# Kernel optimization log

Measured on AMD Instinct MI355X. Metric: run time of the kernel, lower is better.

The kernel has to match this reference:

```python
import jax, jax.numpy as jnp
import numpy as np

D_MODEL = 256
G_CH = 512
N_HEADS = 8
EPS = 1e-6


def setup_inputs() -> dict:
    key0 = jax.random.key(0)
    ks = jax.random.split(key0, 24)
    B, N1, C, G = 2, 65536, D_MODEL, G_CH
    p = 0.05
    inp = {
        'query': jax.random.normal(ks[0], (B, N1, G), jnp.float32),
        'key': jax.random.normal(ks[1], (B, N1, C), jnp.float32),
        'value': jax.random.normal(ks[2], (B, N1, C), jnp.float32),
        # Mheads1: Linear(guidance_channels, d_model, bias=False); stored as [in,out]
        'mheads1_w': jax.random.normal(ks[3], (G, C), jnp.float32) * p,
        # CrossAttentionLayer q/k/v: Linear(d_model, d_model)
        'q_w': jax.random.normal(ks[4], (C, C), jnp.float32) * p,
        'q_b': jax.random.normal(ks[5], (C,), jnp.float32) * p,
        'k_w': jax.random.normal(ks[6], (C, C), jnp.float32) * p,
        'k_b': jax.random.normal(ks[7], (C,), jnp.float32) * p,
        'v_w': jax.random.normal(ks[8], (C, C), jnp.float32) * p,
        'v_b': jax.random.normal(ks[9], (C,), jnp.float32) * p,
        # MSCW local_attn: Linear->ReLU->Linear
        'l1_w': jax.random.normal(ks[10], (C, C), jnp.float32) * p,
        'l1_b': jax.random.normal(ks[11], (C,), jnp.float32) * p,
        'l2_w': jax.random.normal(ks[12], (C, C), jnp.float32) * p,
        'l2_b': jax.random.normal(ks[13], (C,), jnp.float32) * p,
        # MSCW global_attn: Linear->ReLU->Linear
        'g1_w': jax.random.normal(ks[14], (C, C), jnp.float32) * p,
        'g1_b': jax.random.normal(ks[15], (C,), jnp.float32) * p,
        'g2_w': jax.random.normal(ks[16], (C, C), jnp.float32) * p,
        'g2_b': jax.random.normal(ks[17], (C,), jnp.float32) * p,
    }
    return inp


def _haar_pool(feat):
    # feat: [B, C, H, W]; standard WCT2 WavePool: depthwise 2x2 stride-2 Haar conv.
    B, C, H, W = feat.shape
    x = feat.reshape(B, C, H // 2, 2, W // 2, 2)
    a = x[:, :, :, 0, :, 0]
    b = x[:, :, :, 0, :, 1]
    c = x[:, :, :, 1, :, 0]
    d = x[:, :, :, 1, :, 1]
    # Haar: L=[1,1]/sqrt2, Hf=[-1,1]/sqrt2 -> outer-product 2x2 filters, /2 overall
    LL = (a + b + c + d) * 0.5
    LH = (-a + b - c + d) * 0.5
    HL = (-a - b + c + d) * 0.5
    HH = (a - b - c + d) * 0.5
    return LL, LH, HL, HH


def reference(query, key, value, mheads1_w, q_w, q_b, k_w, k_b, v_w, v_b,
              l1_w, l1_b, l2_w, l2_b, g1_w, g1_b, g2_w, g2_b):
    B, n1, C = value.shape
    hw = int(round(n1 ** 0.5))
    q_guid = query @ mheads1_w  # [B, L, C]

    feat = jnp.transpose(key, (0, 2, 1)).reshape(B, C, hw, hw)
    LL, LH, HL, HH = _haar_pool(feat)
    high = HL + LH + HH  # [B, C, hw/2, hw/2]
    low = LL
    high = jnp.transpose(high.reshape(B, C, -1), (0, 2, 1))  # [B, S, C]
    low = jnp.transpose(low.reshape(B, C, -1), (0, 2, 1))

    # MSCW gating
    s = high + low
    pool = jnp.mean(s, axis=1, keepdims=True)
    local = jax.nn.relu(s @ l1_w + l1_b) @ l2_w + l2_b
    glob = jax.nn.relu(pool @ g1_w + g1_b) @ g2_w + g2_b
    wei = jax.nn.sigmoid(local + glob)
    fre = wei * high + low  # [B, S, C]

    # CrossAttentionLayer with linear (elu-feature) attention
    H, Dh = N_HEADS, C // N_HEADS
    qh = (q_guid @ q_w + q_b).reshape(B, -1, H, Dh)
    kh = (fre @ k_w + k_b).reshape(B, -1, H, Dh)
    vh = (fre @ v_w + v_b).reshape(B, -1, H, Dh)
    Q = jax.nn.elu(qh) + 1.0
    K = jax.nn.elu(kh) + 1.0
    S = vh.shape[1]
    Vn = vh / S
    KV = jnp.einsum('nshd,nshv->nhdv', K, Vn)  # [B, H, D, D]
    Z = 1.0 / (jnp.einsum('nlhd,nhd->nlh', Q, K.sum(axis=1)) + EPS)
    out = jnp.einsum('nlhd,nhdv,nlh->nlhv', Q, KV, Z) * S
    return out.reshape(B, -1, C)
```

## Files before the change

kernel.cpp:

```cpp
#include <hip/hip_runtime.h>
#include <math.h>

#define BB 2

#define WS_PPART 0
#define WS_GLOB  66048
#define WS_KVP   66560
#define WS_KSP   590848
#define WS_KVT   607232
#define WS_WFP   619520
#define WS_L1T   685056
#define WS_L2T   717824
#define WS_KWT   750592
#define WS_VWT   783360

typedef __attribute__((ext_vector_type(8))) short short8v;
typedef __attribute__((ext_vector_type(4))) float f32x4;

__device__ __forceinline__ ushort f2bf(float x) {
    union { float f; unsigned int u; } v; v.f = x;
    unsigned int u = v.u;
    unsigned int r = (u + 0x7fffu + ((u >> 16) & 1u)) >> 16;
    return (ushort)r;
}

__device__ __forceinline__ float bf2f(ushort x) {
    union { float f; unsigned int u; } v;
    v.u = ((unsigned int)x) << 16;
    return v.f;
}

__device__ __forceinline__ unsigned int cvtpk(float lo, float hi) {
    unsigned int d;
    asm("v_cvt_pk_bf16_f32 %0, %1, %2" : "=v"(d) : "v"(lo), "v"(hi));
    return d;
}

__device__ __forceinline__ void gload16(const void* g, void* l) {
    __builtin_amdgcn_global_load_lds(
        (const __attribute__((address_space(1))) unsigned int*)g,
        (__attribute__((address_space(3))) unsigned int*)l, 16, 0, 0);
}

__global__ __launch_bounds__(256) void k_prep(const float* __restrict__ l1w, const float* __restrict__ l2w,
                                              const float* __restrict__ kw, const float* __restrict__ vw,
                                              const float* __restrict__ mh, const float* __restrict__ qw,
                                              const float* __restrict__ key,
                                              ushort* __restrict__ t0, ushort* __restrict__ t1,
                                              ushort* __restrict__ t2, ushort* __restrict__ t3,
                                              ushort* __restrict__ wfp, float* __restrict__ ppart) {
    int blk = blockIdx.x, t = threadIdx.x;
    if (blk < 1024) {
        int mat = blk >> 8, k = blk & 255, n = t;
        const float* w = mat == 0 ? l1w : mat == 1 ? l2w : mat == 2 ? kw : vw;
        ushort* o = mat == 0 ? t0 : mat == 1 ? t1 : mat == 2 ? t2 : t3;
        o[(((size_t)(n >> 7) * 8 + (k >> 5)) * 128 + (n & 127)) * 32 + (k & 31)] = f2bf(w[k * 256 + n]);
    } else if (blk < 1536) {
        __shared__ float mr[256];
        int g = blk - 1024;
        mr[t] = mh[g * 256 + t];
        __syncthreads();
        float acc = 0.f;
        for (int k = 0; k < 256; k++) acc += mr[k] * qw[k * 256 + t];
        wfp[(((size_t)(g >> 5) * 256 + t) * 32 + (g & 31))] = f2bf(acc);
    } else {
        int p = blk - 1536;
        int b = p >> 7, ci = p & 127;
        float acc = 0.f;
        for (int q = 0; q < 128; q++) {
            size_t idx = ((size_t)b * 65536 + (size_t)(2 * ci + 1) * 256 + (2 * q + 1)) * 256 + t;
            acc += key[idx];
        }
        ppart[(size_t)p * 256 + t] = acc;
    }
}

__global__ __launch_bounds__(256) void k_glob2(const float* __restrict__ ppart,
                                               const float* __restrict__ g1w,
                                               const float* __restrict__ g1b,
                                               const float* __restrict__ g2w,
                                               const float* __restrict__ g2b,
                                               float* __restrict__ glob) {
    __shared__ float pl[256], hid[256];
    int t = threadIdx.x;
    for (int b = 0; b < BB; b++) {
        float s = 0.f;
        for (int p = 0; p < 128; p++) s += ppart[((size_t)b * 128 + p) * 256 + t];
        pl[t] = s * (2.f / 16384.f);
        __syncthreads();
        float acc = g1b[t];
        for (int k = 0; k < 256; k++) acc += pl[k] * g1w[k * 256 + t];
        hid[t] = fmaxf(acc, 0.f);
        __syncthreads();
        float a2 = g2b[t];
        for (int k = 0; k < 256; k++) a2 += hid[k] * g2w[k * 256 + t];
        glob[b * 256 + t] = a2;
        __syncthreads();
    }
}

template <int AMODE, int EPI>
__global__ __launch_bounds__(256) void gemm_bf(const void* __restrict__ Asrc_,
                                               const ushort* __restrict__ Wt,
                                               const float* __restrict__ bias,
                                               void* __restrict__ Outp,
                                               const float* __restrict__ glob,
                                               const float* __restrict__ key) {
    __shared__ __align__(16) ushort smem[8192];
    ushort* As = smem;
    ushort* Bs = smem + 4096;

    const int tid = threadIdx.x;
    const int lane = tid & 63;
    const int w = tid >> 6;
    const int wrow = w >> 1, wcol = w & 1;
    const int bx = blockIdx.x & 1;
    const int by = blockIdx.x >> 1;
    const int r0 = by * 128, n0 = bx * 128;
    const int l15 = lane & 15, l4 = lane >> 4;

    const int loff = lane * 16;
    char* ldsB0 = (char*)Bs + w * 2048;
    char* ldsB1 = (char*)Bs + w * 2048 + 1024;
    const int rowA0 = w * 32 + (lane >> 2);
    const int kbA = (lane & 3) * 16;
    char* ldsA0 = (char*)As + w * 2048;
    char* ldsA1 = (char*)As + w * 2048 + 1024;
    const int srow = tid >> 1, shalf = tid & 1;
    size_t agbase = 0;
    if constexpr (AMODE == 1) {
        int r = r0 + srow;
        int b = r >> 14, rr = r & 16383;
        int ii = rr >> 7, jj = rr & 127;
        agbase = ((size_t)b * 65536 + (size_t)(2 * ii + 1) * 256 + (2 * jj + 1)) * 256 + shalf * 16;
    }

    f32x4 acc[4][4];
#pragma unroll
    for (int i = 0; i < 4; i++)
#pragma unroll
        for (int j = 0; j < 4; j++) acc[i][j] = (f32x4){0.f, 0.f, 0.f, 0.f};

    for (int ks = 0; ks < 8; ks++) {
        const char* btile = (const char*)Wt + (size_t)(bx * 8 + ks) * 8192;
        gload16(btile + w * 2048 + loff, ldsB0);
        gload16(btile + w * 2048 + 1024 + loff, ldsB1);
        if constexpr (AMODE == 0) {
            const char* ab = (const char*)Asrc_;
            gload16(ab + (size_t)(r0 + rowA0) * 512 + ks * 64 + kbA, ldsA0);
            gload16(ab + (size_t)(r0 + rowA0 + 16) * 512 + ks * 64 + kbA, ldsA1);
        } else {
            const float* kf = (const float*)Asrc_;
            float4 f0 = *(const float4*)(kf + agbase + (size_t)ks * 32);
            float4 f1 = *(const float4*)(kf + agbase + (size_t)ks * 32 + 4);
            float4 f2 = *(const float4*)(kf + agbase + (size_t)ks * 32 + 8);
            float4 f3 = *(const float4*)(kf + agbase + (size_t)ks * 32 + 12);
            uint4 lo = {cvtpk(f0.x * 2.f, f0.y * 2.f), cvtpk(f0.z * 2.f, f0.w * 2.f),
                        cvtpk(f1.x * 2.f, f1.y * 2.f), cvtpk(f1.z * 2.f, f1.w * 2.f)};
            uint4 hi = {cvtpk(f2.x * 2.f, f2.y * 2.f), cvtpk(f2.z * 2.f, f2.w * 2.f),
                        cvtpk(f3.x * 2.f, f3.y * 2.f), cvtpk(f3.z * 2.f, f3.w * 2.f)};
            *(uint4*)((char*)As + srow * 64 + shalf * 32) = lo;
            *(uint4*)((char*)As + srow * 64 + shalf * 32 + 16) = hi;
        }
        __syncthreads();

        short8v a[4], bfr[4];
#pragma unroll
        for (int m = 0; m < 4; m++)
            a[m] = *(const short8v*)((const char*)As + (wrow * 64 + m * 16 + l15) * 64 + l4 * 16);
#pragma unroll
        for (int n = 0; n < 4; n++)
            bfr[n] = *(const short8v*)((const char*)Bs + (wcol * 64 + n * 16 + l15) * 64 + l4 * 16);
#pragma unroll
        for (int m = 0; m < 4; m++)
#pragma unroll
            for (int n = 0; n < 4; n++)
                acc[m][n] = __builtin_amdgcn_mfma_f32_16x16x32_bf16(a[m], bfr[n], acc[m][n], 0, 0, 0);
        __syncthreads();
    }

    const int b = r0 >> 14;
    float bv[4], gv[4];
#pragma unroll
    for (int n = 0; n < 4; n++) {
        int c = n0 + wcol * 64 + n * 16 + l15;
        bv[n] = bias[c];
        if constexpr (EPI == 1) gv[n] = glob[b * 256 + c];
    }
#pragma unroll
    for (int m = 0; m < 4; m++) {
#pragma unroll
        for (int n = 0; n < 4; n++) {
            int c = n0 + wcol * 64 + n * 16 + l15;
#pragma unroll
            for (int r = 0; r < 4; r++) {
                int row = wrow * 64 + m * 16 + l4 * 4 + r;
                int R = r0 + row;
                float x = acc[m][n][r] + bv[n];
                if constexpr (EPI == 0) {
                    ((ushort*)Outp)[(size_t)R * 256 + c] = f2bf(fmaxf(x, 0.f));
                } else if constexpr (EPI == 1) {
                    int rr = R & 16383;
                    int ii = rr >> 7, jj = rr & 127;
                    size_t kb = ((size_t)b * 65536 + (size_t)(2 * ii) * 256 + 2 * jj) * 256 + c;
                    float ka = key[kb];
                    float kb2 = key[kb + 256];
                    float kc2 = key[kb + 65536];
                    float kd2 = key[kb + 65536 + 256];
                    float low = 0.5f * (ka + kb2 + kc2 + kd2);
                    float high = 0.5f * (3.f * kd2 - ka - kb2 - kc2);
                    float wei = 1.f / (1.f + __expf(-(x + gv[n])));
                    ((ushort*)Outp)[(size_t)R * 256 + c] = f2bf(wei * high + low);
                } else if constexpr (EPI == 4) {
                    ((ushort*)Outp)[(size_t)R * 256 + c] = f2bf((x > 0.f) ? x + 1.f : __expf(x));
                } else {
                    ((ushort*)Outp)[(size_t)R * 256 + c] = f2bf(x);
                }
            }
        }
    }
}

__global__ __launch_bounds__(256) void k_kv_part(const ushort* __restrict__ Km,
                                                 const ushort* __restrict__ Vn,
                                                 float* __restrict__ kvp,
                                                 float* __restrict__ ksp) {
    __shared__ float Kl[8][33];
    __shared__ float Vl[8][33];
    int t = threadIdx.x;
    int c = blockIdx.x & 31, h = (blockIdx.x >> 5) & 7, b = blockIdx.x >> 8;
    int d = t >> 3, vq = (t & 7) * 4;
    int lr = t >> 5, lc = t & 31;
    float acc0 = 0, acc1 = 0, acc2 = 0, acc3 = 0, ks = 0;
    size_t rowbase = (size_t)b * 16384 + (size_t)c * 512;
    for (int s0 = 0; s0 < 512; s0 += 8) {
        size_t idx = (rowbase + s0 + lr) * 256 + h * 32 + lc;
        Kl[lr][lc] = bf2f(Km[idx]);
        Vl[lr][lc] = bf2f(Vn[idx]);
        __syncthreads();
#pragma unroll
        for (int rr = 0; rr < 8; rr++) {
            float kd = Kl[rr][d];
            acc0 += kd * Vl[rr][vq];
            acc1 += kd * Vl[rr][vq + 1];
            acc2 += kd * Vl[rr][vq + 2];
            acc3 += kd * Vl[rr][vq + 3];
            ks += kd;
        }
        __syncthreads();
    }
    size_t ob = ((size_t)(b * 8 + h) * 32 + c) * 1024 + d * 32 + vq;
    kvp[ob] = acc0; kvp[ob + 1] = acc1; kvp[ob + 2] = acc2; kvp[ob + 3] = acc3;
    if ((t & 7) == 0) ksp[((b * 8 + h) * 32 + c) * 32 + d] = ks;
}

__global__ __launch_bounds__(256) void k_kv_reduce(const float* __restrict__ kvp,
                                                   const float* __restrict__ ksp,
                                                   ushort* __restrict__ kvt) {
    int bh = blockIdx.x, t = threadIdx.x;
    for (int e = t; e < 1024; e += 256) {
        float s = 0.f;
        for (int cc = 0; cc < 32; cc++) s += kvp[((size_t)bh * 32 + cc) * 1024 + e];
        int d = e >> 5, v = e & 31;
        kvt[((size_t)bh * 48 + v) * 32 + d] = f2bf(s);
    }
    if (t < 32) {
        float s = 0.f;
        for (int cc = 0; cc < 32; cc++) s += ksp[(bh * 32 + cc) * 32 + t];
        kvt[((size_t)bh * 48 + 32) * 32 + t] = f2bf(s);
    }
    for (int z = t; z < 480; z += 256) kvt[(size_t)bh * 48 * 32 + 33 * 32 + z] = 0;
}

__global__ __launch_bounds__(512, 4) void k_qattn_mfma(const float* __restrict__ query,
                                                       const ushort* __restrict__ wfp,
                                                       const float* __restrict__ qb,
                                                       const ushort* __restrict__ kvt,
                                                       float* __restrict__ Out) {
    __shared__ __align__(16) char smem[65536];
    char* As0 = smem;
    char* As1 = smem + 16384;
    char* Bs0 = smem + 32768;
    char* Bs1 = smem + 49152;

    const int tid = threadIdx.x;
    const int lane = tid & 63;
    const int wid = tid >> 6;
    const int wrow = wid >> 2, wcol = wid & 3;
    const int R0 = blockIdx.x * 128;
    const int l15 = lane & 15, l4 = lane >> 4;

    const int arow0 = wid * 16 + (lane >> 3);
    const int achunk = (lane & 7) ^ (lane >> 3);
    const float* aga = query + (size_t)(R0 + arow0) * 512 + achunk * 4;
    const int wb = wid * 2048;
    const int bglo = wb + lane * 16;

    f32x4 acc[4][4];
#pragma unroll
    for (int i = 0; i < 4; i++)
#pragma unroll
        for (int j = 0; j < 4; j++) acc[i][j] = (f32x4){0.f, 0.f, 0.f, 0.f};

#define QSTAGE(dA, dB, kss)                                                     \
    do {                                                                        \
        const float* ga_ = aga + (size_t)(kss) * 32;                            \
        gload16(ga_, (dA) + wb);                                                \
        gload16(ga_ + 8 * 512, (dA) + wb + 1024);                               \
        const char* pan_ = (const char*)wfp + (size_t)(kss) * 16384 + bglo;     \
        gload16(pan_, (dB) + wb);                                               \
        gload16(pan_ + 1024, (dB) + wb + 1024);                                 \
    } while (0)

    QSTAGE(As0, Bs0, 0);
    asm volatile("s_waitcnt vmcnt(0)" ::: "memory");
    __builtin_amdgcn_s_barrier();
    __builtin_amdgcn_sched_barrier(0);

    for (int ks = 0; ks < 16; ks++) {
        const char* bA = (ks & 1) ? As1 : As0;
        const char* bB = (ks & 1) ? Bs1 : Bs0;
        char* nA = (ks & 1) ? As0 : As1;
        char* nB = (ks & 1) ? Bs0 : Bs1;
        if (ks < 15) QSTAGE(nA, nB, ks + 1);

        short8v bfr[4];
#pragma unroll
        for (int n = 0; n < 4; n++)
            bfr[n] = *(const short8v*)(bB + (wcol * 64 + n * 16 + l15) * 64 + l4 * 16);
#pragma unroll
        for (int m = 0; m < 4; m++) {
            int row = wrow * 64 + m * 16 + l15;
            int j0 = (l4 * 2) ^ (l15 & 7);
            const char* rp = bA + row * 128;
            f32x4 lo = *(const f32x4*)(rp + j0 * 16);
            f32x4 hi = *(const f32x4*)(rp + (j0 ^ 1) * 16);
            union { uint4 u; short8v s; } av;
            av.u = (uint4){cvtpk(lo.x, lo.y), cvtpk(lo.z, lo.w),
                           cvtpk(hi.x, hi.y), cvtpk(hi.z, hi.w)};
#pragma unroll
            for (int n = 0; n < 4; n++)
                acc[m][n] = __builtin_amdgcn_mfma_f32_16x16x32_bf16(av.s, bfr[n], acc[m][n], 0, 0, 0);
        }

        if (ks < 15) {
            asm volatile("s_waitcnt vmcnt(0)" ::: "memory");
            __builtin_amdgcn_s_barrier();
            __builtin_amdgcn_sched_barrier(0);
        }
    }
#undef QSTAGE

    __syncthreads();

    float qbv[4];
#pragma unroll
    for (int n = 0; n < 4; n++) qbv[n] = qb[wcol * 64 + n * 16 + l15];
#pragma unroll
    for (int m = 0; m < 4; m++) {
#pragma unroll
        for (int n = 0; n < 4; n++) {
#pragma unroll
            for (int r = 0; r < 4; r++) {
                int rl = m * 16 + l4 * 4 + r;
                int cl = n * 16 + l15;
                float x = acc[m][n][r] + qbv[n];
                float q = x > 0.f ? x + 1.f : __expf(x);
                int byte = wid * 8192 + ((rl * 128 + cl * 2) ^ ((rl & 7) << 4));
                *(ushort*)(smem + byte) = f2bf(q);
            }
        }
    }
    __syncthreads();

    const int bb = R0 >> 16;
#pragma unroll
    for (int hi = 0; hi < 2; hi++) {
        int h = wcol * 2 + hi;
        int bh = bb * 8 + h;
        const ushort* kb = kvt + (size_t)bh * 48 * 32;
        short8v bk0 = *(const short8v*)(kb + (0 * 16 + l15) * 32 + l4 * 8);
        short8v bk1 = *(const short8v*)(kb + (1 * 16 + l15) * 32 + l4 * 8);
        short8v bkz = *(const short8v*)(kb + (2 * 16 + l15) * 32 + l4 * 8);
#pragma unroll
        for (int m = 0; m < 4; m++) {
            int rl = m * 16 + l15;
            int byte = wid * 8192 + ((rl * 128 + hi * 64 + l4 * 16) ^ ((rl & 7) << 4));
            short8v aq = *(const short8v*)(smem + byte);
            f32x4 zero = (f32x4){0.f, 0.f, 0.f, 0.f};
            f32x4 o0 = __builtin_amdgcn_mfma_f32_16x16x32_bf16(aq, bk0, zero, 0, 0, 0);
            f32x4 o1 = __builtin_amdgcn_mfma_f32_16x16x32_bf16(aq, bk1, zero, 0, 0, 0);
            f32x4 oz = __builtin_amdgcn_mfma_f32_16x16x32_bf16(aq, bkz, zero, 0, 0, 0);
#pragma unroll
            for (int r = 0; r < 4; r++) {
                float z = __shfl(oz[r], (lane & 48));
                float sc = 1.f / (z + 1e-6f);
                int grow = R0 + wrow * 64 + m * 16 + l4 * 4 + r;
                int gcol = wcol * 64 + hi * 32 + l15;
                Out[(size_t)grow * 256 + gcol] = o0[r] * sc;
                Out[(size_t)grow * 256 + gcol + 16] = o1[r] * sc;
            }
        }
    }
}

extern "C" void kernel_launch(void* const* d_in, const int* in_sizes, int n_in,
                              void* d_out, int out_size, void* d_ws, size_t ws_size,
                              hipStream_t stream) {
    const float* query = (const float*)d_in[0];
    const float* key = (const float*)d_in[1];
    const float* mh = (const float*)d_in[3];
    const float* q_w = (const float*)d_in[4];
    const float* q_b = (const float*)d_in[5];
    const float* k_w = (const float*)d_in[6];
    const float* k_b = (const float*)d_in[7];
    const float* v_w = (const float*)d_in[8];
    const float* v_b = (const float*)d_in[9];
    const float* l1_w = (const float*)d_in[10];
    const float* l1_b = (const float*)d_in[11];
    const float* l2_w = (const float*)d_in[12];
    const float* l2_b = (const float*)d_in[13];
    const float* g1_w = (const float*)d_in[14];
    const float* g1_b = (const float*)d_in[15];
    const float* g2_w = (const float*)d_in[16];
    const float* g2_b = (const float*)d_in[17];

    float* out = (float*)d_out;
    float* ws = (float*)d_ws;

    float* ppart = ws + WS_PPART;
    float* glob = ws + WS_GLOB;
    float* kvp = ws + WS_KVP;
    float* ksp = ws + WS_KSP;
    ushort* kvt = (ushort*)(ws + WS_KVT);
    ushort* wfp = (ushort*)(ws + WS_WFP);
    ushort* l1t = (ushort*)(ws + WS_L1T);
    ushort* l2t = (ushort*)(ws + WS_L2T);
    ushort* kwt = (ushort*)(ws + WS_KWT);
    ushort* vwt = (ushort*)(ws + WS_VWT);

    ushort* t = (ushort*)out;
    ushort* fre = (ushort*)(out + 4194304);
    ushort* Km = (ushort*)(out + 8388608);
    ushort* Vn = (ushort*)(out + 12582912);

    k_prep<<<1792, 256, 0, stream>>>(l1_w, l2_w, k_w, v_w, mh, q_w, key,
                                     l1t, l2t, kwt, vwt, wfp, ppart);
    k_glob2<<<1, 256, 0, stream>>>(ppart, g1_w, g1_b, g2_w, g2_b, glob);

    gemm_bf<1, 0><<<512, 256, 0, stream>>>(key, l1t, l1_b, t, nullptr, nullptr);
    gemm_bf<0, 1><<<512, 256, 0, stream>>>(t, l2t, l2_b, fre, glob, key);
    gemm_bf<0, 4><<<512, 256, 0, stream>>>(fre, kwt, k_b, Km, nullptr, nullptr);
    gemm_bf<0, 5><<<512, 256, 0, stream>>>(fre, vwt, v_b, Vn, nullptr, nullptr);

    k_kv_part<<<512, 256, 0, stream>>>(Km, Vn, kvp, ksp);
    k_kv_reduce<<<16, 256, 0, stream>>>(kvp, ksp, kvt);

    k_qattn_mfma<<<1024, 512, 0, stream>>>(query, wfp, q_b, kvt, out);
}
```

Measured before the change: 265.6 us.

## Triple-buffer query-projection GEMM pipeline with two stages of prefetch in flight

Replaces the double-buffered LDS pipeline in the query attention MFMA kernel with a three-stage ring buffer, issuing loads two k-steps ahead and waiting only for the oldest stage via a partial vmcnt. This hides more global-load latency behind MFMA work. LDS use grows from 64KB to 96KB, and the launch bound drops from 4 to 2 blocks per CU, which can reduce occupancy.

```diff
diff --git a/kernel.cpp b/kernel.cpp
--- a/kernel.cpp
+++ b/kernel.cpp
@@ -272,16 +272,12 @@
     for (int z = t; z < 480; z += 256) kvt[(size_t)bh * 48 * 32 + 33 * 32 + z] = 0;
 }
 
-__global__ __launch_bounds__(512, 4) void k_qattn_mfma(const float* __restrict__ query,
+__global__ __launch_bounds__(512, 2) void k_qattn_mfma(const float* __restrict__ query,
                                                        const ushort* __restrict__ wfp,
                                                        const float* __restrict__ qb,
                                                        const ushort* __restrict__ kvt,
                                                        float* __restrict__ Out) {
-    __shared__ __align__(16) char smem[65536];
-    char* As0 = smem;
-    char* As1 = smem + 16384;
-    char* Bs0 = smem + 32768;
-    char* Bs1 = smem + 49152;
+    __shared__ __align__(16) char smem[98304];
 
     const int tid = threadIdx.x;
     const int lane = tid & 63;
@@ -302,28 +298,34 @@
 #pragma unroll
         for (int j = 0; j < 4; j++) acc[i][j] = (f32x4){0.f, 0.f, 0.f, 0.f};
 
-#define QSTAGE(dA, dB, kss)                                                     \
+#define QSTAGE(buf, kss)                                                        \
     do {                                                                        \
+        char* dA_ = smem + (buf) * 32768;                                       \
+        char* dB_ = dA_ + 16384;                                                \
         const float* ga_ = aga + (size_t)(kss) * 32;                            \
-        gload16(ga_, (dA) + wb);                                                \
-        gload16(ga_ + 8 * 512, (dA) + wb + 1024);                               \
+        gload16(ga_, dA_ + wb);                                                 \
+        gload16(ga_ + 8 * 512, dA_ + wb + 1024);                                \
         const char* pan_ = (const char*)wfp + (size_t)(kss) * 16384 + bglo;     \
-        gload16(pan_, (dB) + wb);                                               \
-        gload16(pan_ + 1024, (dB) + wb + 1024);                                 \
+        gload16(pan_, dB_ + wb);                                                \
+        gload16(pan_ + 1024, dB_ + wb + 1024);                                  \
     } while (0)
 
-    QSTAGE(As0, Bs0, 0);
-    asm volatile("s_waitcnt vmcnt(0)" ::: "memory");
-    __builtin_amdgcn_s_barrier();
-    __builtin_amdgcn_sched_barrier(0);
-
+    QSTAGE(0, 0);
+    QSTAGE(1, 1);
+
+    int cur = 0, nxt2 = 2;
     for (int ks = 0; ks < 16; ks++) {
-        const char* bA = (ks & 1) ? As1 : As0;
-        const char* bB = (ks & 1) ? Bs1 : Bs0;
-        char* nA = (ks & 1) ? As0 : As1;
-        char* nB = (ks & 1) ? Bs0 : Bs1;
-        if (ks < 15) QSTAGE(nA, nB, ks + 1);
-
+        if (ks < 15) {
+            asm volatile("s_waitcnt vmcnt(4)" ::: "memory");
+        } else {
+            asm volatile("s_waitcnt vmcnt(0)" ::: "memory");
+        }
+        __builtin_amdgcn_s_barrier();
+        __builtin_amdgcn_sched_barrier(0);
+        if (ks + 2 < 16) QSTAGE(nxt2, ks + 2);
+
+        const char* bA = smem + cur * 32768;
+        const char* bB = bA + 16384;
         short8v bfr[4];
 #pragma unroll
         for (int n = 0; n < 4; n++)
@@ -343,11 +345,8 @@
                 acc[m][n] = __builtin_amdgcn_mfma_f32_16x16x32_bf16(av.s, bfr[n], acc[m][n], 0, 0, 0);
         }
 
-        if (ks < 15) {
-            asm volatile("s_waitcnt vmcnt(0)" ::: "memory");
-            __builtin_amdgcn_s_barrier();
-            __builtin_amdgcn_sched_barrier(0);
-        }
+        cur = cur == 2 ? 0 : cur + 1;
+        nxt2 = nxt2 == 2 ? 0 : nxt2 + 1;
     }
 #undef QSTAGE
 
```

Measured after the change: 275.3 us. 3.7% more time.
